# Kernel tuning notes

Measured on AMD Instinct MI355X. Metric: run time of the kernel, lower is better.

The kernel has to match this reference:

```python
import jax, jax.numpy as jnp
import numpy as np
from jax.scipy.special import logsumexp

REG = 0.05
NUM_ITER = 50
N, M, D = 8192, 8192, 128


def _squared_cdist(XP, XQ):
    xx = jnp.sum(XP * XP, axis=1)  # [N]
    yy = jnp.sum(XQ * XQ, axis=1)  # [M]
    C = xx[:, None] + yy[None, :] - 2.0 * (XP @ XQ.T)  # [N, M]
    return jnp.maximum(C, 0.0)


def _sinkhorn_log(a, b, C, reg, n_iter):
    # POT's sinkhorn_log: log-domain potentials u, v; alternating logsumexp updates.
    Mr = -C / reg                      # [N, M]
    loga = jnp.log(a)                  # [N]
    logb = jnp.log(b)                  # [M]

    def body(carry, _):
        u, v = carry
        v = logb - logsumexp(Mr + u[:, None], axis=0)  # column update
        u = loga - logsumexp(Mr + v[None, :], axis=1)  # row update
        return (u, v), None

    init = (jnp.zeros_like(loga), jnp.zeros_like(logb))
    (u, v), _ = jax.lax.scan(body, init, None, length=n_iter)
    return jnp.exp(Mr + u[:, None] + v[None, :])   # transport plan pi [N, M]


def setup_inputs() -> dict:
    key = jax.random.key(0)
    k1, k2 = jax.random.split(key)
    XP = jax.random.normal(k1, (N, D), dtype=jnp.float32)
    XQ = jax.random.normal(k2, (M, D), dtype=jnp.float32)
    return {"XP": XP, "XQ": XQ}


def reference(XP, XQ):
    n, m = XP.shape[0], XQ.shape[0]
    p = jnp.full((n,), 1.0 / n, dtype=XP.dtype)  # unif(len(XP))
    q = jnp.full((m,), 1.0 / m, dtype=XQ.dtype)  # unif(len(XQ))
    C = _squared_cdist(XP, XQ)
    # fit() runs under torch.no_grad() and detaches pi -> stop_gradient
    pi = jax.lax.stop_gradient(_sinkhorn_log(p, q, C, REG, NUM_ITER))
    mapped = (pi / p[:, None]) @ XQ   # barycentric mapping [N, D]
    return mapped, pi
```

## Files before the change

kernel.cpp:

```cpp
#include <hip/hip_runtime.h>


#define NN 8192
#define MMX 8192
#define DD 128
#define NITER 50
#define LOGAB (-9.0109133472792881f)
#define NEG20 (-20.0f)

typedef short bf16x8 __attribute__((ext_vector_type(8)));
typedef float f32x4 __attribute__((ext_vector_type(4)));
typedef unsigned short ushort_t;

static __device__ __forceinline__ void lse_acc(float& m, float& s, float x) {
    float mn = fmaxf(m, x);
    s = s * __expf(m - mn) + __expf(x - mn);
    m = mn;
}
static __device__ __forceinline__ void lse_merge(float& m, float& s, float m2, float s2) {
    float mn = fmaxf(m, m2);
    s = s * __expf(m - mn) + s2 * __expf(m2 - mn);
    m = mn;
}
static __device__ __forceinline__ void lse_acc4(float4& m, float4& s, float4 x) {
    lse_acc(m.x, s.x, x.x);
    lse_acc(m.y, s.y, x.y);
    lse_acc(m.z, s.z, x.z);
    lse_acc(m.w, s.w, x.w);
}
static __device__ __forceinline__ int swz(int r, int k) {
    return k ^ (((r >> 3) & 7) << 2);
}
static __device__ __forceinline__ unsigned f2bf(float x) {
    unsigned u = __float_as_uint(x);
    return (u + 0x7FFF + ((u >> 16) & 1)) >> 16;
}
static __device__ __forceinline__ float4 dec4(uint2 w, float stp, float bas) {
    float4 o;
    o.x = (float)(w.x & 0xFFFFu) * stp + bas;
    o.y = (float)(w.x >> 16)     * stp + bas;
    o.z = (float)(w.y & 0xFFFFu) * stp + bas;
    o.w = (float)(w.y >> 16)     * stp + bas;
    return o;
}

__global__ void k_init(float* u, float* v) {
    int i = blockIdx.x * 1024 + threadIdx.x;
    if (i < 8192) { u[i] = 0.0f; v[i] = 0.0f; }
}

__global__ __launch_bounds__(64) void k_sqnorm(const float* __restrict__ XP,
                                               const float* __restrict__ XQ,
                                               float* __restrict__ xx,
                                               float* __restrict__ yy) {
    int row = blockIdx.x;
    int lane = threadIdx.x;
    const float* src = (row < NN) ? (XP + (size_t)row * DD)
                                  : (XQ + (size_t)(row - NN) * DD);
    float2 w = *(const float2*)&src[lane * 2];
    float sres = w.x * w.x + w.y * w.y;
    #pragma unroll
    for (int off = 32; off > 0; off >>= 1)
        sres += __shfl_down(sres, off, 64);
    if (lane == 0) {
        if (row < NN) xx[row] = sres;
        else          yy[row - NN] = sres;
    }
}

__global__ __launch_bounds__(256) void k_xqt(const float* __restrict__ XQ,
                                             unsigned* __restrict__ XQT32) {
    __shared__ float As[32][129];
    int mb = blockIdx.x * 32;
    int t = threadIdx.x;
    int r = t >> 3, c0 = (t & 7) * 16;
    #pragma unroll
    for (int j = 0; j < 4; ++j)
        *(float4*)&As[r][c0 + j * 4] = *(const float4*)&XQ[(size_t)(mb + r) * DD + c0 + j * 4];
    __syncthreads();
    int d = t >> 1, p0 = (t & 1) * 8;
    #pragma unroll
    for (int j = 0; j < 8; ++j) {
        int pp = p0 + j;
        unsigned lo = f2bf(As[2 * pp][d]);
        unsigned hi = f2bf(As[2 * pp + 1][d]);
        XQT32[(size_t)d * 4096 + (mb >> 1) + pp] = lo | (hi << 16);
    }
}

__global__ __launch_bounds__(256) void k_gemm_mr(const float* __restrict__ XP,
                                                 const float* __restrict__ XQ,
                                                 const float* __restrict__ xx,
                                                 const float* __restrict__ yy,
                                                 float* __restrict__ Mr) {
    __shared__ float As[128][64];
    __shared__ float Bs[128][64];
    int rb = blockIdx.y * 128, cb = blockIdx.x * 128;
    int t = threadIdx.x;
    int ty = t >> 4, tx = t & 15;
    int r0 = ty * 8, c0 = tx * 8;
    float acc[8][8] = {};

    for (int kc = 0; kc < 128; kc += 64) {
        __syncthreads();
        #pragma unroll
        for (int i = 0; i < 8; ++i) {
            int f = i * 256 + t;
            int r = f >> 4;
            int k4 = (f & 15) * 4;
            *(float4*)&As[r][swz(r, k4)] = *(const float4*)&XP[(size_t)(rb + r) * DD + kc + k4];
            *(float4*)&Bs[r][swz(r, k4)] = *(const float4*)&XQ[(size_t)(cb + r) * DD + kc + k4];
        }
        __syncthreads();
        for (int k = 0; k < 64; k += 4) {
            float4 a[8], b[8];
            #pragma unroll
            for (int i = 0; i < 8; ++i) {
                a[i] = *(float4*)&As[r0 + i][swz(r0 + i, k)];
                b[i] = *(float4*)&Bs[c0 + i][swz(c0 + i, k)];
            }
            #pragma unroll
            for (int i = 0; i < 8; ++i)
                #pragma unroll
                for (int j = 0; j < 8; ++j)
                    acc[i][j] += a[i].x * b[j].x + a[i].y * b[j].y +
                                 a[i].z * b[j].z + a[i].w * b[j].w;
        }
    }

    float yv[8];
    *(float4*)&yv[0] = *(const float4*)&yy[cb + c0];
    *(float4*)&yv[4] = *(const float4*)&yy[cb + c0 + 4];
    #pragma unroll
    for (int i = 0; i < 8; ++i) {
        int gr = rb + r0 + i;
        float xxi = xx[gr];
        float4 o0, o1;
        o0.x = NEG20 * fmaxf(xxi + yv[0] - 2.f * acc[i][0], 0.f);
        o0.y = NEG20 * fmaxf(xxi + yv[1] - 2.f * acc[i][1], 0.f);
        o0.z = NEG20 * fmaxf(xxi + yv[2] - 2.f * acc[i][2], 0.f);
        o0.w = NEG20 * fmaxf(xxi + yv[3] - 2.f * acc[i][3], 0.f);
        o1.x = NEG20 * fmaxf(xxi + yv[4] - 2.f * acc[i][4], 0.f);
        o1.y = NEG20 * fmaxf(xxi + yv[5] - 2.f * acc[i][5], 0.f);
        o1.z = NEG20 * fmaxf(xxi + yv[6] - 2.f * acc[i][6], 0.f);
        o1.w = NEG20 * fmaxf(xxi + yv[7] - 2.f * acc[i][7], 0.f);
        *(float4*)&Mr[(size_t)gr * MMX + cb + c0] = o0;
        *(float4*)&Mr[(size_t)gr * MMX + cb + c0 + 4] = o1;
    }
}

__global__ __launch_bounds__(256) void k_quant(float* __restrict__ Mr) {
    float* slot = Mr + (size_t)blockIdx.x * MMX;
    int t = threadIdx.x;
    float4 x[8];
    float mn = 1e30f, mx = -1e30f;
    #pragma unroll
    for (int i = 0; i < 8; ++i) {
        x[i] = *(const float4*)&slot[(t + 256 * i) * 4];
        mn = fminf(mn, fminf(fminf(x[i].x, x[i].y), fminf(x[i].z, x[i].w)));
        mx = fmaxf(mx, fmaxf(fmaxf(x[i].x, x[i].y), fmaxf(x[i].z, x[i].w)));
    }
    #pragma unroll
    for (int off = 32; off > 0; off >>= 1) {
        mn = fminf(mn, __shfl_xor(mn, off));
        mx = fmaxf(mx, __shfl_xor(mx, off));
    }
    __shared__ float smn[4], smx[4];
    int wid = t >> 6;
    if ((t & 63) == 0) { smn[wid] = mn; smx[wid] = mx; }
    __syncthreads();
    mn = fminf(fminf(smn[0], smn[1]), fminf(smn[2], smn[3]));
    mx = fmaxf(fmaxf(smx[0], smx[1]), fmaxf(smx[2], smx[3]));
    float span = fmaxf(mx - mn, 1e-20f);
    float inv = 65535.0f / span;
    float stp = span * (1.0f / 65535.0f);
    uint2* out16 = (uint2*)slot;
    #pragma unroll
    for (int i = 0; i < 8; ++i) {
        unsigned q0 = (unsigned)fminf(rintf((x[i].x - mn) * inv), 65535.f);
        unsigned q1 = (unsigned)fminf(rintf((x[i].y - mn) * inv), 65535.f);
        unsigned q2 = (unsigned)fminf(rintf((x[i].z - mn) * inv), 65535.f);
        unsigned q3 = (unsigned)fminf(rintf((x[i].w - mn) * inv), 65535.f);
        out16[t + 256 * i] = make_uint2(q0 | (q1 << 16), q2 | (q3 << 16));
    }
    if (t == 0) *(float2*)&slot[4096] = make_float2(mn, stp);
}

__global__ __launch_bounds__(256) void k_colpass_q(const float* __restrict__ Mr,
                                                   const float* __restrict__ u,
                                                   float* __restrict__ part) {
    int c = blockIdx.x * 1024 + threadIdx.x * 4;
    int n0 = blockIdx.y * 128;
    float4 mx = make_float4(-1e30f, -1e30f, -1e30f, -1e30f);
    float4 s = make_float4(0.f, 0.f, 0.f, 0.f);
    #pragma unroll 4
    for (int r = 0; r < 128; ++r) {
        const float* slot = Mr + (size_t)(n0 + r) * MMX;
        float2 bs = *(const float2*)&slot[4096];
        float basu = bs.x + u[n0 + r];
        uint2 w = *(const uint2*)((const ushort_t*)slot + c);
        lse_acc4(mx, s, dec4(w, bs.y, basu));
    }
    float4 o;
    o.x = mx.x + __logf(s.x);
    o.y = mx.y + __logf(s.y);
    o.z = mx.z + __logf(s.z);
    o.w = mx.w + __logf(s.w);
    *(float4*)&part[(size_t)blockIdx.y * MMX + c] = o;
}

__global__ __launch_bounds__(256) void k_colpass(const float* __restrict__ Mr,
                                                 const float* __restrict__ u,
                                                 float* __restrict__ part) {
    int c = blockIdx.x * 1024 + threadIdx.x * 4;
    int n0 = blockIdx.y * 128;
    float4 mx = make_float4(-1e30f, -1e30f, -1e30f, -1e30f);
    float4 s = make_float4(0.f, 0.f, 0.f, 0.f);
    #pragma unroll 8
    for (int r = 0; r < 128; ++r) {
        float un = u[n0 + r];
        float4 w = *(const float4*)&Mr[(size_t)(n0 + r) * MMX + c];
        w.x += un; w.y += un; w.z += un; w.w += un;
        lse_acc4(mx, s, w);
    }
    float4 o;
    o.x = mx.x + __logf(s.x);
    o.y = mx.y + __logf(s.y);
    o.z = mx.z + __logf(s.z);
    o.w = mx.w + __logf(s.w);
    *(float4*)&part[(size_t)blockIdx.y * MMX + c] = o;
}

__global__ __launch_bounds__(256) void k_colcombine(const float* __restrict__ part,
                                                    float* __restrict__ v) {
    int m = blockIdx.x * 256 + threadIdx.x;
    float mx = -1e30f, s = 0.f;
    #pragma unroll 8
    for (int ch = 0; ch < 64; ++ch)
        lse_acc(mx, s, part[(size_t)ch * MMX + m]);
    v[m] = LOGAB - (mx + __logf(s));
}

__global__ __launch_bounds__(256) void k_rowpass_q(const float* __restrict__ Mr,
                                                   const float* __restrict__ v,
                                                   float* __restrict__ u) {
    int n0 = blockIdx.x * 8;
    int t = threadIdx.x;
    float basr[8], stpr[8];
    const ushort_t* us[8];
    #pragma unroll
    for (int r = 0; r < 8; ++r) {
        const float* slot = Mr + (size_t)(n0 + r) * MMX;
        float2 bs = *(const float2*)&slot[4096];
        basr[r] = bs.x;
        stpr[r] = bs.y;
        us[r] = (const ushort_t*)slot;
    }
    float4 mx[8], s[8];
    #pragma unroll
    for (int r = 0; r < 8; ++r) {
        mx[r] = make_float4(-1e30f, -1e30f, -1e30f, -1e30f);
        s[r] = make_float4(0.f, 0.f, 0.f, 0.f);
    }
    const float4* v4 = (const float4*)v;
    for (int i = t; i < MMX / 4; i += 256) {
        float4 vv = v4[i];
        #pragma unroll
        for (int r = 0; r < 8; ++r) {
            uint2 w = *(const uint2*)&us[r][i * 4];
            float4 d = dec4(w, stpr[r], basr[r]);
            d.x += vv.x; d.y += vv.y; d.z += vv.z; d.w += vv.w;
            lse_acc4(mx[r], s[r], d);
        }
    }
    __shared__ float smm[8][4], sss[8][4];
    int wid = t >> 6, lane = t & 63;
    #pragma unroll
    for (int r = 0; r < 8; ++r) {
        float m1 = mx[r].x, s1 = s[r].x;
        lse_merge(m1, s1, mx[r].y, s[r].y);
        lse_merge(m1, s1, mx[r].z, s[r].z);
        lse_merge(m1, s1, mx[r].w, s[r].w);
        #pragma unroll
        for (int off = 32; off > 0; off >>= 1) {
            float m2 = __shfl_xor(m1, off);
            float s2 = __shfl_xor(s1, off);
            lse_merge(m1, s1, m2, s2);
        }
        if (lane == 0) { smm[r][wid] = m1; sss[r][wid] = s1; }
    }
    __syncthreads();
    if (t < 8) {
        float m1 = smm[t][0], s1 = sss[t][0];
        lse_merge(m1, s1, smm[t][1], sss[t][1]);
        lse_merge(m1, s1, smm[t][2], sss[t][2]);
        lse_merge(m1, s1, smm[t][3], sss[t][3]);
        u[n0 + t] = LOGAB - (m1 + __logf(s1));
    }
}

__global__ __launch_bounds__(256) void k_rowpass(const float* __restrict__ Mr,
                                                 const float* __restrict__ v,
                                                 float* __restrict__ u) {
    int n0 = blockIdx.x * 8;
    int t = threadIdx.x;
    float4 mx[8], s[8];
    #pragma unroll
    for (int r = 0; r < 8; ++r) {
        mx[r] = make_float4(-1e30f, -1e30f, -1e30f, -1e30f);
        s[r] = make_float4(0.f, 0.f, 0.f, 0.f);
    }
    const float4* v4 = (const float4*)v;
    for (int i = t; i < MMX / 4; i += 256) {
        float4 vv = v4[i];
        #pragma unroll
        for (int r = 0; r < 8; ++r) {
            float4 w = *(const float4*)&Mr[(size_t)(n0 + r) * MMX + i * 4];
            w.x += vv.x; w.y += vv.y; w.z += vv.z; w.w += vv.w;
            lse_acc4(mx[r], s[r], w);
        }
    }
    __shared__ float smm[8][4], sss[8][4];
    int wid = t >> 6, lane = t & 63;
    #pragma unroll
    for (int r = 0; r < 8; ++r) {
        float m1 = mx[r].x, s1 = s[r].x;
        lse_merge(m1, s1, mx[r].y, s[r].y);
        lse_merge(m1, s1, mx[r].z, s[r].z);
        lse_merge(m1, s1, mx[r].w, s[r].w);
        #pragma unroll
        for (int off = 32; off > 0; off >>= 1) {
            float m2 = __shfl_xor(m1, off);
            float s2 = __shfl_xor(s1, off);
            lse_merge(m1, s1, m2, s2);
        }
        if (lane == 0) { smm[r][wid] = m1; sss[r][wid] = s1; }
    }
    __syncthreads();
    if (t < 8) {
        float m1 = smm[t][0], s1 = sss[t][0];
        lse_merge(m1, s1, smm[t][1], sss[t][1]);
        lse_merge(m1, s1, smm[t][2], sss[t][2]);
        lse_merge(m1, s1, smm[t][3], sss[t][3]);
        u[n0 + t] = LOGAB - (m1 + __logf(s1));
    }
}

__global__ __launch_bounds__(512, 1) void k_pi_mapped_mfma_q(float* __restrict__ P,
                                                             const unsigned* __restrict__ XQT32,
                                                             const float* __restrict__ u,
                                                             const float* __restrict__ v,
                                                             float* __restrict__ mapped) {
    __shared__ unsigned short PIs[32 * 64];
    __shared__ unsigned short QTs[128 * 64];
    int r0 = blockIdx.x * 32;
    int t = threadIdx.x;
    int wid = t >> 6, lane = t & 63;
    int ntile = (wid >> 2) * 16;
    int dbase = (wid & 3) * 32;
    int prow = t >> 4;
    int pm4 = (t & 15) * 4;
    int pgran = (t & 15) >> 1, phalf = t & 1;
    int qd = t >> 2;
    int qg0 = (t & 3) * 2;

    float* slotp = P + (size_t)(r0 + prow) * MMX;
    const ushort_t* usp = (const ushort_t*)slotp;
    float2 bs = *(const float2*)&slotp[4096];
    float stp = bs.y;
    float basu = bs.x + u[r0 + prow];

    f32x4 acc[2];
    acc[0] = (f32x4)(0.f);
    acc[1] = (f32x4)(0.f);

    int mb0 = MMX - 64;
    uint2 pq = *(const uint2*)&usp[mb0 + pm4];
    float4 vv = *(const float4*)&v[mb0 + pm4];
    uint4 xa = *(const uint4*)&XQT32[(size_t)qd * 4096 + (mb0 >> 1) + qg0 * 4];
    uint4 xb = *(const uint4*)&XQT32[(size_t)qd * 4096 + (mb0 >> 1) + qg0 * 4 + 4];

    for (int mb = mb0; mb >= 0; mb -= 64) {
        __syncthreads();
        float4 d = dec4(pq, stp, basu);
        float4 w;
        w.x = __expf(d.x + vv.x);
        w.y = __expf(d.y + vv.y);
        w.z = __expf(d.z + vv.z);
        w.w = __expf(d.w + vv.w);
        uint2 pk;
        pk.x = f2bf(w.x) | (f2bf(w.y) << 16);
        pk.y = f2bf(w.z) | (f2bf(w.w) << 16);
        *(uint2*)&PIs[prow * 64 + (((pgran ^ (prow & 7)) * 16 + phalf * 8) >> 1)] = pk;
        *(uint4*)&QTs[qd * 64 + (((qg0 ^ (qd & 7)) * 16) >> 1)] = xa;
        *(uint4*)&QTs[qd * 64 + ((((qg0 + 1) ^ (qd & 7)) * 16) >> 1)] = xb;
        __syncthreads();
        *(float4*)&slotp[mb + pm4] = w;
        if (mb > 0) {
            int nb = mb - 64;
            pq = *(const uint2*)&usp[nb + pm4];
            vv = *(const float4*)&v[nb + pm4];
            xa = *(const uint4*)&XQT32[(size_t)qd * 4096 + (nb >> 1) + qg0 * 4];
            xb = *(const uint4*)&XQT32[(size_t)qd * 4096 + (nb >> 1) + qg0 * 4 + 4];
        }
        int arow = ntile + (lane & 15);
        bf16x8 afr[2];
        #pragma unroll
        for (int ks = 0; ks < 2; ++ks) {
            int g = ks * 4 + (lane >> 4);
            afr[ks] = *(bf16x8*)&PIs[arow * 64 + (((g ^ (arow & 7)) * 16) >> 1)];
        }
        #pragma unroll
        for (int dt = 0; dt < 2; ++dt) {
            int drow = dbase + dt * 16 + (lane & 15);
            #pragma unroll
            for (int ks = 0; ks < 2; ++ks) {
                int g = ks * 4 + (lane >> 4);
                bf16x8 bfr = *(bf16x8*)&QTs[drow * 64 + (((g ^ (drow & 7)) * 16) >> 1)];
                acc[dt] = __builtin_amdgcn_mfma_f32_16x16x32_bf16(afr[ks], bfr, acc[dt], 0, 0, 0);
            }
        }
    }
    #pragma unroll
    for (int dt = 0; dt < 2; ++dt) {
        int dcol = dbase + dt * 16 + (lane & 15);
        #pragma unroll
        for (int reg = 0; reg < 4; ++reg) {
            int nrow = r0 + ntile + (lane >> 4) * 4 + reg;
            mapped[(size_t)nrow * DD + dcol] = acc[dt][reg] * 8192.f;
        }
    }
}

__global__ __launch_bounds__(512, 1) void k_pi_mapped(float* __restrict__ P,
                                                      const float* __restrict__ XQ,
                                                      const float* __restrict__ u,
                                                      const float* __restrict__ v,
                                                      float* __restrict__ mapped) {
    __shared__ float PIs[32][68];
    __shared__ float QS[64][128];
    int r0 = blockIdx.x * 32;
    int t = threadIdx.x;
    int tid = t & 255;
    int half = t >> 8;
    int rg = tid >> 5;
    int dg = tid & 31;
    int prow = t >> 4;
    int pc4 = (t & 15) * 4;
    int qrb = t >> 5;
    int qc4 = (t & 31) * 4;
    float urow = u[r0 + prow];

    float4 acc[4];
    acc[0] = acc[1] = acc[2] = acc[3] = make_float4(0.f, 0.f, 0.f, 0.f);

    float4 pw, vv, xq0, xq1, xq2, xq3;
    pw = *(const float4*)&P[(size_t)(r0 + prow) * MMX + pc4];
    vv = *(const float4*)&v[pc4];
    xq0 = *(const float4*)&XQ[(size_t)(qrb) * DD + qc4];
    xq1 = *(const float4*)&XQ[(size_t)(16 + qrb) * DD + qc4];
    xq2 = *(const float4*)&XQ[(size_t)(32 + qrb) * DD + qc4];
    xq3 = *(const float4*)&XQ[(size_t)(48 + qrb) * DD + qc4];

    for (int mb = 0; mb < MMX; mb += 64) {
        __syncthreads();
        float4 w;
        w.x = __expf(pw.x + urow + vv.x);
        w.y = __expf(pw.y + urow + vv.y);
        w.z = __expf(pw.z + urow + vv.z);
        w.w = __expf(pw.w + urow + vv.w);
        *(float4*)&PIs[prow][pc4] = w;
        *(float4*)&QS[qrb][qc4] = xq0;
        *(float4*)&QS[16 + qrb][qc4] = xq1;
        *(float4*)&QS[32 + qrb][qc4] = xq2;
        *(float4*)&QS[48 + qrb][qc4] = xq3;
        __syncthreads();
        *(float4*)&P[(size_t)(r0 + prow) * MMX + mb + pc4] = w;
        if (mb + 64 < MMX) {
            int nb = mb + 64;
            pw = *(const float4*)&P[(size_t)(r0 + prow) * MMX + nb + pc4];
            vv = *(const float4*)&v[nb + pc4];
            xq0 = *(const float4*)&XQ[(size_t)(nb + qrb) * DD + qc4];
            xq1 = *(const float4*)&XQ[(size_t)(nb + 16 + qrb) * DD + qc4];
            xq2 = *(const float4*)&XQ[(size_t)(nb + 32 + qrb) * DD + qc4];
            xq3 = *(const float4*)&XQ[(size_t)(nb + 48 + qrb) * DD + qc4];
        }
        #pragma unroll
        for (int sstep = 0; sstep < 8; ++sstep) {
            int k = (half * 8 + sstep) * 4;
            float4 q0 = *(float4*)&QS[k + 0][dg * 4];
            float4 q1 = *(float4*)&QS[k + 1][dg * 4];
            float4 q2 = *(float4*)&QS[k + 2][dg * 4];
            float4 q3 = *(float4*)&QS[k + 3][dg * 4];
            #pragma unroll
            for (int j = 0; j < 4; ++j) {
                float4 p = *(float4*)&PIs[rg * 4 + j][k];
                acc[j].x += p.x * q0.x + p.y * q1.x + p.z * q2.x + p.w * q3.x;
                acc[j].y += p.x * q0.y + p.y * q1.y + p.z * q2.y + p.w * q3.y;
                acc[j].z += p.x * q0.z + p.y * q1.z + p.z * q2.z + p.w * q3.z;
                acc[j].w += p.x * q0.w + p.y * q1.w + p.z * q2.w + p.w * q3.w;
            }
        }
    }
    __syncthreads();
    float* mrg = &QS[0][0];
    if (half == 1) {
        #pragma unroll
        for (int j = 0; j < 4; ++j)
            *(float4*)&mrg[tid * 16 + j * 4] = acc[j];
    }
    __syncthreads();
    if (half == 0) {
        #pragma unroll
        for (int j = 0; j < 4; ++j) {
            float4 o = *(const float4*)&mrg[tid * 16 + j * 4];
            o.x = (acc[j].x + o.x) * 8192.f;
            o.y = (acc[j].y + o.y) * 8192.f;
            o.z = (acc[j].z + o.z) * 8192.f;
            o.w = (acc[j].w + o.w) * 8192.f;
            *(float4*)&mapped[(size_t)(r0 + rg * 4 + j) * DD + dg * 4] = o;
        }
    }
}

__global__ __launch_bounds__(256) void k_pi(float* __restrict__ Mr,
                                            const float* __restrict__ u,
                                            const float* __restrict__ v) {
    const float4* v4 = (const float4*)v;
    for (int i = blockIdx.x * 256 + threadIdx.x; i < NN * MMX / 4; i += 2048 * 256) {
        int n = i >> 11;
        int m4 = i & 2047;
        float un = u[n];
        float4 vv = v4[m4];
        float4* p = (float4*)Mr + i;
        float4 w = *p;
        w.x = __expf(w.x + un + vv.x);
        w.y = __expf(w.y + un + vv.y);
        w.z = __expf(w.z + un + vv.z);
        w.w = __expf(w.w + un + vv.w);
        *p = w;
    }
}

__global__ __launch_bounds__(256) void k_mapped(const float* __restrict__ pi,
                                                const float* __restrict__ XQ,
                                                float* __restrict__ mapped) {
    __shared__ float XQs[64][128];
    __shared__ float PIs[32][64];
    int r0 = blockIdx.x * 32;
    int t = threadIdx.x;
    int dg = (t & 31) * 4;
    int rg = (t >> 5) * 4;
    float4 acc[4];
    #pragma unroll
    for (int j = 0; j < 4; ++j) acc[j] = make_float4(0.f, 0.f, 0.f, 0.f);

    for (int mb = 0; mb < MMX; mb += 64) {
        __syncthreads();
        #pragma unroll
        for (int i = 0; i < 8; ++i) {
            int f = i * 256 + t;
            int rr = f >> 5;
            int k4 = (f & 31) * 4;
            *(float4*)&XQs[rr][k4] = *(const float4*)&XQ[(size_t)(mb + rr) * DD + k4];
        }
        #pragma unroll
        for (int i = 0; i < 2; ++i) {
            int f = i * 256 + t;
            int rr = f >> 4;
            int c4 = (f & 15) * 4;
            *(float4*)&PIs[rr][c4] = *(const float4*)&pi[(size_t)(r0 + rr) * MMX + mb + c4];
        }
        __syncthreads();
        for (int mm = 0; mm < 64; mm += 4) {
            float4 q0 = *(float4*)&XQs[mm + 0][dg];
            float4 q1 = *(float4*)&XQs[mm + 1][dg];
            float4 q2 = *(float4*)&XQs[mm + 2][dg];
            float4 q3 = *(float4*)&XQs[mm + 3][dg];
            #pragma unroll
            for (int j = 0; j < 4; ++j) {
                float4 p = *(float4*)&PIs[rg + j][mm];
                acc[j].x += p.x * q0.x + p.y * q1.x + p.z * q2.x + p.w * q3.x;
                acc[j].y += p.x * q0.y + p.y * q1.y + p.z * q2.y + p.w * q3.y;
                acc[j].z += p.x * q0.z + p.y * q1.z + p.z * q2.z + p.w * q3.z;
                acc[j].w += p.x * q0.w + p.y * q1.w + p.z * q2.w + p.w * q3.w;
            }
        }
    }
    #pragma unroll
    for (int j = 0; j < 4; ++j) {
        float4 o = acc[j];
        o.x *= 8192.f; o.y *= 8192.f; o.z *= 8192.f; o.w *= 8192.f;
        *(float4*)&mapped[(size_t)(r0 + rg + j) * DD + dg] = o;
    }
}

extern "C" void kernel_launch(void* const* d_in, const int* in_sizes, int n_in,
                              void* d_out, int out_size, void* d_ws, size_t ws_size,
                              hipStream_t stream) {
    const float* XP = (const float*)d_in[0];
    const float* XQ = (const float*)d_in[1];
    float* out = (float*)d_out;
    float* Mr = out + (size_t)NN * DD;
    float* part = out + 65536;

    bool big = (ws_size >= 2228224);
    bool mid = (ws_size >= 131072);
    unsigned* XQT32 = big ? (unsigned*)d_ws : nullptr;
    float* wsf = big ? (float*)((char*)d_ws + 2097152) : (float*)d_ws;
    float* u  = mid ? wsf           : out;
    float* v  = mid ? wsf + 8192    : out + 8192;
    float* xx = mid ? wsf + 16384   : out + 40960;
    float* yy = mid ? wsf + 24576   : out + 49152;

    k_init<<<8, 1024, 0, stream>>>(u, v);
    k_sqnorm<<<NN + MMX, 64, 0, stream>>>(XP, XQ, xx, yy);
    k_gemm_mr<<<dim3(64, 64), 256, 0, stream>>>(XP, XQ, xx, yy, Mr);
    if (big) {
        k_xqt<<<256, 256, 0, stream>>>(XQ, XQT32);
        k_quant<<<8192, 256, 0, stream>>>(Mr);
    }

    for (int it = 0; it < NITER; ++it) {
        if (big) {
            k_colpass_q<<<dim3(8, 64), 256, 0, stream>>>(Mr, u, part);
            k_colcombine<<<32, 256, 0, stream>>>(part, v);
            k_rowpass_q<<<1024, 256, 0, stream>>>(Mr, v, u);
        } else {
            k_colpass<<<dim3(8, 64), 256, 0, stream>>>(Mr, u, part);
            k_colcombine<<<32, 256, 0, stream>>>(part, v);
            k_rowpass<<<1024, 256, 0, stream>>>(Mr, v, u);
        }
    }

    if (big) {
        k_pi_mapped_mfma_q<<<256, 512, 0, stream>>>(Mr, XQT32, u, v, out);
    } else if (mid) {
        k_pi_mapped<<<256, 512, 0, stream>>>(Mr, XQ, u, v, out);
    } else {
        k_pi<<<2048, 256, 0, stream>>>(Mr, u, v);
        k_mapped<<<256, 256, 0, stream>>>(Mr, XQ, out);
    }
}
```

Baseline: 4.378 ms.

## Use split-bf16 MFMA for cost GEMM and finer column-pass row split

```diff
diff --git a/kernel.cpp b/kernel.cpp
--- a/kernel.cpp
+++ b/kernel.cpp
@@ -42,6 +42,15 @@
     o.z = (float)(w.y & 0xFFFFu) * stp + bas;
     o.w = (float)(w.y >> 16)     * stp + bas;
     return o;
+}
+static __device__ __forceinline__ uint2 packhl(float4 x, uint2& lo) {
+    unsigned h0 = f2bf(x.x), h1 = f2bf(x.y), h2 = f2bf(x.z), h3 = f2bf(x.w);
+    float r0 = x.x - __uint_as_float(h0 << 16);
+    float r1 = x.y - __uint_as_float(h1 << 16);
+    float r2 = x.z - __uint_as_float(h2 << 16);
+    float r3 = x.w - __uint_as_float(h3 << 16);
+    lo = make_uint2(f2bf(r0) | (f2bf(r1) << 16), f2bf(r2) | (f2bf(r3) << 16));
+    return make_uint2(h0 | (h1 << 16), h2 | (h3 << 16));
 }
 
 __global__ void k_init(float* u, float* v) {
@@ -86,6 +95,85 @@
         unsigned hi = f2bf(As[2 * pp + 1][d]);
         XQT32[(size_t)d * 4096 + (mb >> 1) + pp] = lo | (hi << 16);
     }
+}
+
+__global__ __launch_bounds__(256, 2) void k_gemm_mr_mfma(const float* __restrict__ XP,
+                                                         const float* __restrict__ XQ,
+                                                         const float* __restrict__ xx,
+                                                         const float* __restrict__ yy,
+                                                         float* __restrict__ Mr) {
+    __shared__ ushort_t Ah[128 * 64], Al[128 * 64];
+    __shared__ ushort_t Bh[128 * 64], Bl[128 * 64];
+    int rb = blockIdx.y * 128, cb = blockIdx.x * 128;
+    int t = threadIdx.x;
+    int w = t >> 6, lane = t & 63;
+    int lane15 = lane & 15, lhi = lane >> 4;
+    int wr = (w >> 1) * 64, wc = (w & 1) * 64;
+
+    f32x4 acc00 = (f32x4)(0.f), acc01 = acc00, acc02 = acc00, acc03 = acc00;
+    f32x4 acc10 = acc00, acc11 = acc00, acc12 = acc00, acc13 = acc00;
+    f32x4 acc20 = acc00, acc21 = acc00, acc22 = acc00, acc23 = acc00;
+    f32x4 acc30 = acc00, acc31 = acc00, acc32 = acc00, acc33 = acc00;
+
+    for (int kc = 0; kc < 128; kc += 64) {
+        __syncthreads();
+        #pragma unroll
+        for (int i = 0; i < 8; ++i) {
+            int f = i * 256 + t;
+            int r = f >> 4;
+            int k4 = (f & 15) * 4;
+            int g = k4 >> 3, hf = (k4 >> 2) & 1;
+            int wa = r * 64 + ((g ^ (r & 7)) * 8 + hf * 4);
+            float4 a = *(const float4*)&XP[(size_t)(rb + r) * DD + kc + k4];
+            float4 b = *(const float4*)&XQ[(size_t)(cb + r) * DD + kc + k4];
+            uint2 alo, blo;
+            uint2 ahi = packhl(a, alo);
+            uint2 bhi = packhl(b, blo);
+            *(uint2*)&Ah[wa] = ahi; *(uint2*)&Al[wa] = alo;
+            *(uint2*)&Bh[wa] = bhi; *(uint2*)&Bl[wa] = blo;
+        }
+        __syncthreads();
+        #pragma unroll
+        for (int ks = 0; ks < 2; ++ks) {
+            int g = ks * 4 + lhi;
+            bf16x8 ah[4], al[4], bh[4], bl[4];
+            #pragma unroll
+            for (int i = 0; i < 4; ++i) {
+                int ar = wr + i * 16 + lane15;
+                int ao = ar * 64 + ((g ^ (ar & 7)) * 8);
+                ah[i] = *(bf16x8*)&Ah[ao];
+                al[i] = *(bf16x8*)&Al[ao];
+                int br = wc + i * 16 + lane15;
+                int bo = br * 64 + ((g ^ (br & 7)) * 8);
+                bh[i] = *(bf16x8*)&Bh[bo];
+                bl[i] = *(bf16x8*)&Bl[bo];
+            }
+            #define MM3(AC, I, J) \
+                AC = __builtin_amdgcn_mfma_f32_16x16x32_bf16(ah[I], bh[J], AC, 0, 0, 0); \
+                AC = __builtin_amdgcn_mfma_f32_16x16x32_bf16(ah[I], bl[J], AC, 0, 0, 0); \
+                AC = __builtin_amdgcn_mfma_f32_16x16x32_bf16(al[I], bh[J], AC, 0, 0, 0);
+            MM3(acc00,0,0) MM3(acc01,0,1) MM3(acc02,0,2) MM3(acc03,0,3)
+            MM3(acc10,1,0) MM3(acc11,1,1) MM3(acc12,1,2) MM3(acc13,1,3)
+            MM3(acc20,2,0) MM3(acc21,2,1) MM3(acc22,2,2) MM3(acc23,2,3)
+            MM3(acc30,3,0) MM3(acc31,3,1) MM3(acc32,3,2) MM3(acc33,3,3)
+            #undef MM3
+        }
+    }
+    float yv[4];
+    #pragma unroll
+    for (int j = 0; j < 4; ++j) yv[j] = yy[cb + wc + j * 16 + lane15];
+    #define EPI(AC, I, J) { \
+        _Pragma("unroll") \
+        for (int reg = 0; reg < 4; ++reg) { \
+            int gr = rb + wr + I * 16 + lhi * 4 + reg; \
+            float C = xx[gr] + yv[J] - 2.f * AC[reg]; \
+            Mr[(size_t)gr * MMX + cb + wc + J * 16 + lane15] = NEG20 * fmaxf(C, 0.f); \
+        } }
+    EPI(acc00,0,0) EPI(acc01,0,1) EPI(acc02,0,2) EPI(acc03,0,3)
+    EPI(acc10,1,0) EPI(acc11,1,1) EPI(acc12,1,2) EPI(acc13,1,3)
+    EPI(acc20,2,0) EPI(acc21,2,1) EPI(acc22,2,2) EPI(acc23,2,3)
+    EPI(acc30,3,0) EPI(acc31,3,1) EPI(acc32,3,2) EPI(acc33,3,3)
+    #undef EPI
 }
 
 __global__ __launch_bounds__(256) void k_gemm_mr(const float* __restrict__ XP,
@@ -186,15 +274,15 @@
     if (t == 0) *(float2*)&slot[4096] = make_float2(mn, stp);
 }
 
-__global__ __launch_bounds__(256) void k_colpass_q(const float* __restrict__ Mr,
-                                                   const float* __restrict__ u,
-                                                   float* __restrict__ part) {
+__global__ __launch_bounds__(256) void k_colpass_q64(const float* __restrict__ Mr,
+                                                     const float* __restrict__ u,
+                                                     float* __restrict__ part) {
     int c = blockIdx.x * 1024 + threadIdx.x * 4;
-    int n0 = blockIdx.y * 128;
+    int n0 = blockIdx.y * 64;
     float4 mx = make_float4(-1e30f, -1e30f, -1e30f, -1e30f);
     float4 s = make_float4(0.f, 0.f, 0.f, 0.f);
-    #pragma unroll 4
-    for (int r = 0; r < 128; ++r) {
+    #pragma unroll 8
+    for (int r = 0; r < 64; ++r) {
         const float* slot = Mr + (size_t)(n0 + r) * MMX;
         float2 bs = *(const float2*)&slot[4096];
         float basu = bs.x + u[n0 + r];
@@ -207,6 +295,24 @@
     o.z = mx.z + __logf(s.z);
     o.w = mx.w + __logf(s.w);
     *(float4*)&part[(size_t)blockIdx.y * MMX + c] = o;
+}
+
+__global__ __launch_bounds__(256) void k_colcombine128(const float* __restrict__ part,
+                                                       float* __restrict__ v) {
+    int t = threadIdx.x;
+    int col = blockIdx.x * 128 + (t & 127);
+    int half = t >> 7;
+    float mx = -1e30f, s = 0.f;
+    #pragma unroll 8
+    for (int ch = 0; ch < 64; ++ch)
+        lse_acc(mx, s, part[(size_t)(half * 64 + ch) * MMX + col]);
+    __shared__ float sm[256];
+    if (half) { sm[t & 127] = mx; sm[128 + (t & 127)] = s; }
+    __syncthreads();
+    if (!half) {
+        lse_merge(mx, s, sm[t], sm[128 + t]);
+        v[col] = LOGAB - (mx + __logf(s));
+    }
 }
 
 __global__ __launch_bounds__(256) void k_colpass(const float* __restrict__ Mr,
@@ -602,7 +708,6 @@
     const float* XQ = (const float*)d_in[1];
     float* out = (float*)d_out;
     float* Mr = out + (size_t)NN * DD;
-    float* part = out + 65536;
 
     bool big = (ws_size >= 2228224);
     bool mid = (ws_size >= 131072);
@@ -612,23 +717,27 @@
     float* v  = mid ? wsf + 8192    : out + 8192;
     float* xx = mid ? wsf + 16384   : out + 40960;
     float* yy = mid ? wsf + 24576   : out + 49152;
+    float* part_big = out;
+    float* part_mid = out + 65536;
 
     k_init<<<8, 1024, 0, stream>>>(u, v);
     k_sqnorm<<<NN + MMX, 64, 0, stream>>>(XP, XQ, xx, yy);
-    k_gemm_mr<<<dim3(64, 64), 256, 0, stream>>>(XP, XQ, xx, yy, Mr);
     if (big) {
+        k_gemm_mr_mfma<<<dim3(64, 64), 256, 0, stream>>>(XP, XQ, xx, yy, Mr);
         k_xqt<<<256, 256, 0, stream>>>(XQ, XQT32);
         k_quant<<<8192, 256, 0, stream>>>(Mr);
+    } else {
+        k_gemm_mr<<<dim3(64, 64), 256, 0, stream>>>(XP, XQ, xx, yy, Mr);
     }
 
     for (int it = 0; it < NITER; ++it) {
         if (big) {
-            k_colpass_q<<<dim3(8, 64), 256, 0, stream>>>(Mr, u, part);
-            k_colcombine<<<32, 256, 0, stream>>>(part, v);
+            k_colpass_q64<<<dim3(8, 128), 256, 0, stream>>>(Mr, u, part_big);
+            k_colcombine128<<<64, 256, 0, stream>>>(part_big, v);
             k_rowpass_q<<<1024, 256, 0, stream>>>(Mr, v, u);
         } else {
-            k_colpass<<<dim3(8, 64), 256, 0, stream>>>(Mr, u, part);
-            k_colcombine<<<32, 256, 0, stream>>>(part, v);
+            k_colpass<<<dim3(8, 64), 256, 0, stream>>>(Mr, u, part_mid);
+            k_colcombine<<<32, 256, 0, stream>>>(part_mid, v);
             k_rowpass<<<1024, 256, 0, stream>>>(Mr, v, u);
         }
     }
```

Measured after the change: 4.022 ms. 8.1% less time.
